# Kernel optimization log

Hardware: AMD Instinct MI355X
Metric: run time of the kernel (lower is better)

Reference implementation:

```python
import jax, jax.numpy as jnp
import numpy as np

SPATIAL_SHAPES = [(80, 80), (40, 40), (20, 20)]  # (h, w) per level; sum(h*w) = 8400


def setup_inputs() -> dict:
    key = jax.random.key(0)
    k1, k2, k3 = jax.random.split(key, 3)
    bs, Lv, nH, c = 16, 8400, 8, 32
    Lq, L, P = 300, 3, 4
    value = jax.random.normal(k1, (bs, Lv, nH, c), dtype=jnp.float32)
    value_spatial_shapes = jnp.asarray(SPATIAL_SHAPES, dtype=jnp.int64)
    sampling_locations = jax.random.uniform(k2, (bs, Lq, nH, L, P, 2), dtype=jnp.float32)
    aw = jax.random.uniform(k3, (bs, Lq, nH, L, P), dtype=jnp.float32)
    attention_weights = aw / jnp.sum(aw, axis=(-2, -1), keepdims=True)
    return {
        "value": value,
        "value_spatial_shapes": value_spatial_shapes,
        "sampling_locations": sampling_locations,
        "attention_weights": attention_weights,
    }


def _sample_level(v, g, h, w):
    """Bilinear zero-padded sampling (grid_sample, align_corners=False).
    v: [bs, h*w, nH, c] (row-major h,w); g: [bs, Lq, nH, P, 2] in [0,1].
    Returns [bs, Lq, P, nH, c]."""
    bs, _, nH, c = v.shape
    Lq, P = g.shape[1], g.shape[3]
    # grid_sample align_corners=False: pixel = ((2*loc-1 + 1)*size - 1)/2 = loc*size - 0.5
    x = g[..., 0] * w - 0.5  # [bs, Lq, nH, P]
    y = g[..., 1] * h - 0.5
    x0 = jnp.floor(x)
    y0 = jnp.floor(y)
    acc = jnp.zeros((bs, Lq, P, nH, c), dtype=v.dtype)
    for dx in (0, 1):
        for dy in (0, 1):
            xi = x0 + dx
            yi = y0 + dy
            wgt = (1.0 - jnp.abs(x - xi)) * (1.0 - jnp.abs(y - yi))
            valid = (xi >= 0) & (xi < w) & (yi >= 0) & (yi < h)
            wgt = jnp.where(valid, wgt, 0.0)  # zero padding
            xc = jnp.clip(xi, 0, w - 1).astype(jnp.int32)
            yc = jnp.clip(yi, 0, h - 1).astype(jnp.int32)
            idx = yc * w + xc  # [bs, Lq, nH, P]
            idx = jnp.transpose(idx, (0, 1, 3, 2)).reshape(bs, Lq * P, nH, 1)
            gathered = jnp.take_along_axis(v, idx, axis=1)  # [bs, Lq*P, nH, c]
            gathered = gathered.reshape(bs, Lq, P, nH, c)
            wgt_t = jnp.transpose(wgt, (0, 1, 3, 2))  # [bs, Lq, P, nH]
            acc = acc + gathered * wgt_t[..., None]
    return acc


def reference(value, value_spatial_shapes, sampling_locations, attention_weights):
    # value_spatial_shapes is static metadata (used for shapes) -> host ints
    shapes = [(int(h), int(w)) for h, w in np.asarray(value_spatial_shapes)]
    bs, _, nH, c = value.shape
    Lq = sampling_locations.shape[1]
    splits = np.cumsum([h * w for h, w in shapes])[:-1]
    value_list = jnp.split(value, splits, axis=1)
    sampled = []
    for lvl, (h, w) in enumerate(shapes):
        g = sampling_locations[:, :, :, lvl]  # [bs, Lq, nH, P, 2]
        sampled.append(_sample_level(value_list[lvl], g, h, w))
    stacked = jnp.stack(sampled, axis=2)  # [bs, Lq, L, P, nH, c]
    out = jnp.einsum('bqlpnc,bqnlp->bqnc', stacked, attention_weights)
    return out.reshape(bs, Lq, nH * c)
```

## Files before the change

### kernel.cpp

```cpp
#include <hip/hip_runtime.h>

#define BS   16
#define LQ   300
#define NH   8
#define C    32
#define NLVL 3
#define NPT  4
#define LV   8400
#define PH_STRIDE (NH * (C / 4))

__global__ __launch_bounds__(256) void msda_fwd(
    const float* __restrict__ value,
    const float* __restrict__ loc,
    const float* __restrict__ attw,
    float* __restrict__ out)
{
    const int tid = blockIdx.x * blockDim.x + threadIdx.x;
    const int c4 = tid & 7;
    const int h  = (tid >> 3) & (NH - 1);
    const int bq = tid >> 6;
    if (bq >= BS * LQ) return;
    const int b = bq / LQ;

    const float* lp = loc  + (size_t)(bq * NH + h) * (NLVL * NPT * 2);
    const float* ap = attw + (size_t)(bq * NH + h) * (NLVL * NPT);

    const float4* vb = (const float4*)value
                     + ((size_t)b * LV) * PH_STRIDE + h * (C / 4) + c4;

    float4 acc = make_float4(0.f, 0.f, 0.f, 0.f);

    const int Hs[NLVL] = {80, 40, 20};
    const int Ws[NLVL] = {80, 40, 20};
    const int Os[NLVL] = {0, 6400, 8000};

    #pragma unroll
    for (int l = 0; l < NLVL; ++l) {
        const int H = Hs[l], W = Ws[l];
        const float4* vl = vb + (size_t)Os[l] * PH_STRIDE;
        #pragma unroll
        for (int p = 0; p < NPT; ++p) {
            const float gx = lp[(l * NPT + p) * 2 + 0];
            const float gy = lp[(l * NPT + p) * 2 + 1];
            const float aw = ap[l * NPT + p];

            const float x = gx * (float)W - 0.5f;
            const float y = gy * (float)H - 0.5f;
            const float xf = floorf(x), yf = floorf(y);
            const int x0 = (int)xf, y0 = (int)yf;
            const int x1 = x0 + 1,  y1 = y0 + 1;
            const float lx = x - xf, ly = y - yf;
            const float hx = 1.f - lx, hy = 1.f - ly;

            float w00 = hx * hy * aw;
            float w10 = lx * hy * aw;
            float w01 = hx * ly * aw;
            float w11 = lx * ly * aw;

            const bool vx0 = (unsigned)x0 < (unsigned)W;
            const bool vx1 = (unsigned)x1 < (unsigned)W;
            const bool vy0 = (unsigned)y0 < (unsigned)H;
            const bool vy1 = (unsigned)y1 < (unsigned)H;
            w00 = (vx0 && vy0) ? w00 : 0.f;
            w10 = (vx1 && vy0) ? w10 : 0.f;
            w01 = (vx0 && vy1) ? w01 : 0.f;
            w11 = (vx1 && vy1) ? w11 : 0.f;

            const int xc0 = min(max(x0, 0), W - 1);
            const int xc1 = min(max(x1, 0), W - 1);
            const int yc0 = min(max(y0, 0), H - 1);
            const int yc1 = min(max(y1, 0), H - 1);

            const float4 v00 = vl[(size_t)(yc0 * W + xc0) * PH_STRIDE];
            const float4 v10 = vl[(size_t)(yc0 * W + xc1) * PH_STRIDE];
            const float4 v01 = vl[(size_t)(yc1 * W + xc0) * PH_STRIDE];
            const float4 v11 = vl[(size_t)(yc1 * W + xc1) * PH_STRIDE];

            acc.x += v00.x * w00 + v10.x * w10 + v01.x * w01 + v11.x * w11;
            acc.y += v00.y * w00 + v10.y * w10 + v01.y * w01 + v11.y * w11;
            acc.z += v00.z * w00 + v10.z * w10 + v01.z * w01 + v11.z * w11;
            acc.w += v00.w * w00 + v10.w * w10 + v01.w * w01 + v11.w * w11;
        }
    }

    ((float4*)out)[(size_t)(bq * NH + h) * (C / 4) + c4] = acc;
}

extern "C" void kernel_launch(void* const* d_in, const int* in_sizes, int n_in,
                              void* d_out, int out_size, void* d_ws, size_t ws_size,
                              hipStream_t stream) {
    const float* value = (const float*)d_in[0];
    const float* loc   = (const float*)d_in[2];
    const float* attw  = (const float*)d_in[3];
    float* out = (float*)d_out;

    const int total = BS * LQ * NH * (C / 4);
    const int block = 256;
    const int grid  = (total + block - 1) / block;
    msda_fwd<<<grid, block, 0, stream>>>(value, loc, attw, out);
}
```

Before: 198.0 us.

## Split sampling points across four thread groups and reduce partial sums in LDS

Each block now handles one (batch, query) pair. Its 256 threads are split into four groups of 64, and each group samples 3 of the 12 level/point samples. The groups write partial sums to shared memory, and after a barrier 64 threads combine them. This gives four times as many threads, which means more memory requests in flight to hide gather latency. In exchange it adds an LDS reduction, a __syncthreads, and idle threads during the final step. It also sets launch_bounds to occupancy 4 and uses byte-offset addressing with shifts.

Result: faster. 194.0 us (median of 2 runs) (-2.0%).

```diff
diff --git a/kernel.cpp b/kernel.cpp
--- a/kernel.cpp
+++ b/kernel.cpp
@@ -4,86 +4,103 @@
 #define LQ   300
 #define NH   8
 #define C    32
-#define NLVL 3
-#define NPT  4
 #define LV   8400
-#define PH_STRIDE (NH * (C / 4))
+#define POS_BYTES 1024
 
-__global__ __launch_bounds__(256) void msda_fwd(
+__device__ __forceinline__ void sample_point(
+    const char* __restrict__ vbase, float gx, float gy, float aw,
+    int W, int H, int off, float4& acc)
+{
+    const float x = gx * (float)W - 0.5f;
+    const float y = gy * (float)H - 0.5f;
+    const float xf = floorf(x), yf = floorf(y);
+    const int x0 = (int)xf, y0 = (int)yf;
+    const int x1 = x0 + 1,  y1 = y0 + 1;
+    const float lx = x - xf, ly = y - yf;
+    const float hx = 1.f - lx, hy = 1.f - ly;
+
+    float w00 = hx * hy * aw;
+    float w10 = lx * hy * aw;
+    float w01 = hx * ly * aw;
+    float w11 = lx * ly * aw;
+
+    const bool vx0 = (unsigned)x0 < (unsigned)W;
+    const bool vx1 = (unsigned)x1 < (unsigned)W;
+    const bool vy0 = (unsigned)y0 < (unsigned)H;
+    const bool vy1 = (unsigned)y1 < (unsigned)H;
+    w00 = (vx0 && vy0) ? w00 : 0.f;
+    w10 = (vx1 && vy0) ? w10 : 0.f;
+    w01 = (vx0 && vy1) ? w01 : 0.f;
+    w11 = (vx1 && vy1) ? w11 : 0.f;
+
+    const int xc0 = min(max(x0, 0), W - 1);
+    const int xc1 = min(max(x1, 0), W - 1);
+    const int yc0 = min(max(y0, 0), H - 1);
+    const int yc1 = min(max(y1, 0), H - 1);
+
+    const int r0 = off + yc0 * W;
+    const int r1 = off + yc1 * W;
+    const float4 v00 = *(const float4*)(vbase + ((r0 + xc0) << 10));
+    const float4 v10 = *(const float4*)(vbase + ((r0 + xc1) << 10));
+    const float4 v01 = *(const float4*)(vbase + ((r1 + xc0) << 10));
+    const float4 v11 = *(const float4*)(vbase + ((r1 + xc1) << 10));
+
+    acc.x += v00.x * w00 + v10.x * w10 + v01.x * w01 + v11.x * w11;
+    acc.y += v00.y * w00 + v10.y * w10 + v01.y * w01 + v11.y * w11;
+    acc.z += v00.z * w00 + v10.z * w10 + v01.z * w01 + v11.z * w11;
+    acc.w += v00.w * w00 + v10.w * w10 + v01.w * w01 + v11.w * w11;
+}
+
+__global__ __launch_bounds__(256, 4) void msda_fwd(
     const float* __restrict__ value,
     const float* __restrict__ loc,
     const float* __restrict__ attw,
     float* __restrict__ out)
 {
-    const int tid = blockIdx.x * blockDim.x + threadIdx.x;
-    const int c4 = tid & 7;
-    const int h  = (tid >> 3) & (NH - 1);
-    const int bq = tid >> 6;
-    if (bq >= BS * LQ) return;
-    const int b = bq / LQ;
+    __shared__ float4 lds[256];
 
-    const float* lp = loc  + (size_t)(bq * NH + h) * (NLVL * NPT * 2);
-    const float* ap = attw + (size_t)(bq * NH + h) * (NLVL * NPT);
+    const int t  = threadIdx.x;
+    const int bq = blockIdx.x;
+    const int c4 = t & 7;
+    const int h  = (t >> 3) & (NH - 1);
+    const int pg = t >> 6;
+    const int b  = bq / LQ;
 
-    const float4* vb = (const float4*)value
-                     + ((size_t)b * LV) * PH_STRIDE + h * (C / 4) + c4;
+    const float2* lp = (const float2*)(loc + (size_t)(bq * NH + h) * 24);
+    const float*  ap = attw + (size_t)(bq * NH + h) * 12;
+    const char* vbase = (const char*)value
+                      + (size_t)b * LV * POS_BYTES + h * (C * 4) + c4 * 16;
 
     float4 acc = make_float4(0.f, 0.f, 0.f, 0.f);
 
-    const int Hs[NLVL] = {80, 40, 20};
-    const int Ws[NLVL] = {80, 40, 20};
-    const int Os[NLVL] = {0, 6400, 8000};
+#define SAMPLE(i, W_, H_, OFF_) do {                         \
+        const float2 g = lp[i];                              \
+        sample_point(vbase, g.x, g.y, ap[i], W_, H_, OFF_, acc); \
+    } while (0)
 
-    #pragma unroll
-    for (int l = 0; l < NLVL; ++l) {
-        const int H = Hs[l], W = Ws[l];
-        const float4* vl = vb + (size_t)Os[l] * PH_STRIDE;
-        #pragma unroll
-        for (int p = 0; p < NPT; ++p) {
-            const float gx = lp[(l * NPT + p) * 2 + 0];
-            const float gy = lp[(l * NPT + p) * 2 + 1];
-            const float aw = ap[l * NPT + p];
+    switch (pg) {
+    case 0: SAMPLE(0, 80, 80, 0);    SAMPLE(1, 80, 80, 0);    SAMPLE(2,  80, 80, 0);    break;
+    case 1: SAMPLE(3, 80, 80, 0);    SAMPLE(4, 40, 40, 6400); SAMPLE(5,  40, 40, 6400); break;
+    case 2: SAMPLE(6, 40, 40, 6400); SAMPLE(7, 40, 40, 6400); SAMPLE(8,  20, 20, 8000); break;
+    default:SAMPLE(9, 20, 20, 8000); SAMPLE(10,20, 20, 8000); SAMPLE(11, 20, 20, 8000); break;
+    }
+#undef SAMPLE
 
-            const float x = gx * (float)W - 0.5f;
-            const float y = gy * (float)H - 0.5f;
-            const float xf = floorf(x), yf = floorf(y);
-            const int x0 = (int)xf, y0 = (int)yf;
-            const int x1 = x0 + 1,  y1 = y0 + 1;
-            const float lx = x - xf, ly = y - yf;
-            const float hx = 1.f - lx, hy = 1.f - ly;
+    lds[t] = acc;
+    __syncthreads();
 
-            float w00 = hx * hy * aw;
-            float w10 = lx * hy * aw;
-            float w01 = hx * ly * aw;
-            float w11 = lx * ly * aw;
-
-            const bool vx0 = (unsigned)x0 < (unsigned)W;
-            const bool vx1 = (unsigned)x1 < (unsigned)W;
-            const bool vy0 = (unsigned)y0 < (unsigned)H;
-            const bool vy1 = (unsigned)y1 < (unsigned)H;
-            w00 = (vx0 && vy0) ? w00 : 0.f;
-            w10 = (vx1 && vy0) ? w10 : 0.f;
-            w01 = (vx0 && vy1) ? w01 : 0.f;
-            w11 = (vx1 && vy1) ? w11 : 0.f;
-
-            const int xc0 = min(max(x0, 0), W - 1);
-            const int xc1 = min(max(x1, 0), W - 1);
-            const int yc0 = min(max(y0, 0), H - 1);
-            const int yc1 = min(max(y1, 0), H - 1);
-
-            const float4 v00 = vl[(size_t)(yc0 * W + xc0) * PH_STRIDE];
-            const float4 v10 = vl[(size_t)(yc0 * W + xc1) * PH_STRIDE];
-            const float4 v01 = vl[(size_t)(yc1 * W + xc0) * PH_STRIDE];
-            const float4 v11 = vl[(size_t)(yc1 * W + xc1) * PH_STRIDE];
-
-            acc.x += v00.x * w00 + v10.x * w10 + v01.x * w01 + v11.x * w11;
-            acc.y += v00.y * w00 + v10.y * w10 + v01.y * w01 + v11.y * w11;
-            acc.z += v00.z * w00 + v10.z * w10 + v01.z * w01 + v11.z * w11;
-            acc.w += v00.w * w00 + v10.w * w10 + v01.w * w01 + v11.w * w11;
-        }
+    if (t < 64) {
+        float4 a0 = lds[t];
+        float4 a1 = lds[t + 64];
+        float4 a2 = lds[t + 128];
+        float4 a3 = lds[t + 192];
+        float4 r;
+        r.x = (a0.x + a1.x) + (a2.x + a3.x);
+        r.y = (a0.y + a1.y) + (a2.y + a3.y);
+        r.z = (a0.z + a1.z) + (a2.z + a3.z);
+        r.w = (a0.w + a1.w) + (a2.w + a3.w);
+        ((float4*)out)[(size_t)bq * 64 + t] = r;
     }
-
-    ((float4*)out)[(size_t)(bq * NH + h) * (C / 4) + c4] = acc;
 }
 
 extern "C" void kernel_launch(void* const* d_in, const int* in_sizes, int n_in,
@@ -94,8 +111,6 @@
     const float* attw  = (const float*)d_in[3];
     float* out = (float*)d_out;
 
-    const int total = BS * LQ * NH * (C / 4);
-    const int block = 256;
-    const int grid  = (total + block - 1) / block;
-    msda_fwd<<<grid, block, 0, stream>>>(value, loc, attw, out);
+    const int grid = BS * LQ;
+    msda_fwd<<<grid, 256, 0, stream>>>(value, loc, attw, out);
 }
```
